# Kernel optimization log

Hardware: AMD Instinct MI355X
Metric: run time of the kernel (lower is better)

## Reference

```python
import jax, jax.numpy as jnp
import numpy as np

N = 50000      # nodes
E = 800000     # edges
F_IN = 128     # input_dim
H = 4          # GAT heads
C = 32         # hidden_dim (per head)
HC = H * C     # 128, concat GAT output
NG = 64        # graphs in batch
OUT = 10       # classes


def _gat_conv(x, src, dst, W, att_src, att_dst, bias):
    # PyG GATConv (concat=True, add_self_loops=True, negative_slope=0.2)
    n = x.shape[0]
    h = (x @ W).reshape(n, H, -1)                      # [N,H,C]
    a_s = (h * att_src).sum(-1)                        # [N,H]
    a_d = (h * att_dst).sum(-1)                        # [N,H]
    loop = jnp.arange(n)
    s = jnp.concatenate([src, loop])                   # self-loops appended
    d = jnp.concatenate([dst, loop])
    e = jax.nn.leaky_relu(a_s[s] + a_d[d], 0.2)        # [E+N,H]
    m = jax.ops.segment_max(e, d, num_segments=n)
    e = jnp.exp(e - m[d])
    z = jax.ops.segment_sum(e, d, num_segments=n)
    alpha = e / (z[d] + 1e-16)                         # edge softmax per dst,head
    out = jax.ops.segment_sum(h[s] * alpha[..., None], d, num_segments=n)
    return out.reshape(n, -1) + bias                   # [N,H*C]


def setup_inputs() -> dict:
    key = jax.random.key(0)
    ks = jax.random.split(key, 20)
    g = lambda k, shp, fan: jax.random.normal(k, shp, jnp.float32) / np.sqrt(fan)
    inp = {
        'x': jax.random.normal(ks[0], (N, F_IN), jnp.float32),
        'edge_index': jax.random.randint(ks[1], (2, E), 0, N),
        'batch': jnp.sort(jax.random.randint(ks[2], (N,), 0, NG)),
        # GATConv 1: F_IN -> H*C
        'W1': g(ks[3], (F_IN, HC), F_IN),
        'as1': g(ks[4], (H, C), C), 'ad1': g(ks[5], (H, C), C),
        'b1': jnp.zeros((HC,), jnp.float32),
        # GATConv 2: H*C -> H*C
        'W2': g(ks[6], (HC, HC), HC),
        'as2': g(ks[7], (H, C), C), 'ad2': g(ks[8], (H, C), C),
        'b2': jnp.zeros((HC,), jnp.float32),
        # GraphConv: H*C -> C  (lin_rel has bias, lin_root does not)
        'W3r': g(ks[9], (HC, C), HC), 'W3l': g(ks[10], (HC, C), HC),
        'b3': jnp.zeros((C,), jnp.float32),
        # SAGEConv: C -> C (mean aggr; lin_l has bias, lin_r does not)
        'W4l': g(ks[11], (C, C), C), 'b4l': jnp.zeros((C,), jnp.float32),
        'W4r': g(ks[12], (C, C), C),
        # MLP head
        'Wf1': g(ks[13], (C, C), C), 'bf1': jnp.zeros((C,), jnp.float32),
        'Wf2': g(ks[14], (C, OUT), C), 'bf2': jnp.zeros((OUT,), jnp.float32),
    }
    return inp


def reference(x, edge_index, batch, W1, as1, ad1, b1, W2, as2, ad2, b2,
              W3r, W3l, b3, W4l, b4l, W4r, Wf1, bf1, Wf2, bf2):
    src, dst = edge_index[0], edge_index[1]
    relu = jax.nn.relu
    n = x.shape[0]
    # GAT layers (dropout is identity in eval)
    x = relu(_gat_conv(x, src, dst, W1, as1, ad1, b1))
    x = relu(_gat_conv(x, src, dst, W2, as2, ad2, b2))
    # GraphConv: lin_rel(sum_neighbors) + lin_root(x)
    agg = jax.ops.segment_sum(x[src], dst, num_segments=n)
    x = relu(agg @ W3r + b3 + x @ W3l)
    # SAGEConv: lin_l(mean_neighbors) + lin_r(x)
    deg = jax.ops.segment_sum(jnp.ones((src.shape[0],), x.dtype), dst, num_segments=n)
    mean = jax.ops.segment_sum(x[src], dst, num_segments=n) / jnp.maximum(deg, 1.0)[:, None]
    x = relu(mean @ W4l + b4l + x @ W4r)
    # global mean pool over graphs
    cnt = jax.ops.segment_sum(jnp.ones((n,), x.dtype), batch, num_segments=NG)
    gpool = jax.ops.segment_sum(x, batch, num_segments=NG) / jnp.maximum(cnt, 1.0)[:, None]
    gpool = relu(gpool @ Wf1 + bf1)
    return gpool @ Wf2 + bf2
```

## Files before the change

### kernel.cpp

```cpp
#include <hip/hip_runtime.h>
#include <hip/hip_bf16.h>
#include <type_traits>


typedef __bf16 v8bf __attribute__((ext_vector_type(8)));
typedef float  v4f  __attribute__((ext_vector_type(4)));

__device__ __forceinline__ float lrelu(float x) { return x > 0.f ? x : 0.2f * x; }

__device__ __forceinline__ unsigned short f2bf(float f) {
    unsigned u = __float_as_uint(f);
    unsigned r = (u + 0x7FFF + ((u >> 16) & 1)) >> 16;
    return (unsigned short)r;
}
__device__ __forceinline__ float bfbits2f(unsigned short u) {
    return __uint_as_float((unsigned)u << 16);
}
__device__ __forceinline__ float bflo(int v) { return __uint_as_float((unsigned)v << 16); }
__device__ __forceinline__ float bfhi(int v) { return __uint_as_float((unsigned)v & 0xffff0000u); }
__device__ __forceinline__ int packbf2(float a, float b) {
    return (int)f2bf(a) | ((int)f2bf(b) << 16);
}

__device__ __forceinline__ void fma8(float* acc, int4 u, float w) {
    acc[0] += w * bflo(u.x); acc[1] += w * bfhi(u.x);
    acc[2] += w * bflo(u.y); acc[3] += w * bfhi(u.y);
    acc[4] += w * bflo(u.z); acc[5] += w * bfhi(u.z);
    acc[6] += w * bflo(u.w); acc[7] += w * bfhi(u.w);
}


__global__ __launch_bounds__(256) void bucket_hist(const int* __restrict__ dst,
                                                   int* __restrict__ bcount,
                                                   int E, int nbuck) {
    __shared__ int hist[256];
    int t = threadIdx.x;
    for (int i = t; i < nbuck; i += 256) hist[i] = 0;
    __syncthreads();
    int base = blockIdx.x * 4096;
    #pragma unroll
    for (int k = 0; k < 16; ++k) {
        int e = base + k * 256 + t;
        if (e < E) atomicAdd(&hist[dst[e] >> 8], 1);
    }
    __syncthreads();
    for (int i = t; i < nbuck; i += 256) {
        int c = hist[i];
        if (c) atomicAdd(&bcount[i], c);
    }
}

__global__ __launch_bounds__(256) void scan_convert(
    const int* __restrict__ bcount, int* __restrict__ bbase, int* __restrict__ gcursor,
    int nbuck, int E, int* __restrict__ rowptr, int n,
    const float* __restrict__ W1, const float* __restrict__ W2,
    const float* __restrict__ W3r, const float* __restrict__ W3l,
    const float* __restrict__ as1, const float* __restrict__ ad1,
    const float* __restrict__ as2, const float* __restrict__ ad2,
    __hip_bfloat16* __restrict__ W1t, __hip_bfloat16* __restrict__ W2t,
    __hip_bfloat16* __restrict__ W3rt, __hip_bfloat16* __restrict__ W3lt)
{
    int t = threadIdx.x;
    if (blockIdx.x == 0) {
        __shared__ int red[256];
        int v = (t < nbuck) ? bcount[t] : 0;
        red[t] = v;
        __syncthreads();
        for (int off = 1; off < 256; off <<= 1) {
            int u = (t >= off) ? red[t - off] : 0;
            __syncthreads();
            red[t] += u;
            __syncthreads();
        }
        int ex = red[t] - v;
        if (t < nbuck) { bbase[t] = ex; gcursor[t] = ex; }
        if (t == 0) { bbase[nbuck] = E; rowptr[n] = E; }
        return;
    }
    int b = blockIdx.x - 1;
    int i = b * 256 + t;
    {
        int k = i >> 7, c = i & 127;
        *(unsigned short*)&W1t[c * 128 + k] = f2bf(W1[i]);
        *(unsigned short*)&W2t[c * 128 + k] = f2bf(W2[i]);
    }
    if (i < 4096) {
        int k = i >> 5, c = i & 31;
        *(unsigned short*)&W3rt[c * 128 + k] = f2bf(W3r[i]);
        *(unsigned short*)&W3lt[c * 128 + k] = f2bf(W3l[i]);
    }
    if (b == 0) {
        for (int u = t; u < 512; u += 256) {
            int k = u & 127, hd = u >> 7;
            float vs1 = 0.f, vd1 = 0.f, vs2 = 0.f, vd2 = 0.f;
            #pragma unroll
            for (int j = 0; j < 32; ++j) {
                int c = hd * 32 + j;
                float w1 = W1[k * 128 + c], w2 = W2[k * 128 + c];
                vs1 += w1 * as1[c]; vd1 += w1 * ad1[c];
                vs2 += w2 * as2[c]; vd2 += w2 * ad2[c];
            }
            unsigned short h1s = f2bf(vs1), h1d = f2bf(vd1);
            unsigned short h2s = f2bf(vs2), h2d = f2bf(vd2);
            *(unsigned short*)&W1t[(128 + hd) * 128 + k] = h1s;
            *(unsigned short*)&W1t[(132 + hd) * 128 + k] = f2bf(vs1 - bfbits2f(h1s));
            *(unsigned short*)&W1t[(136 + hd) * 128 + k] = h1d;
            *(unsigned short*)&W1t[(140 + hd) * 128 + k] = f2bf(vd1 - bfbits2f(h1d));
            *(unsigned short*)&W2t[(128 + hd) * 128 + k] = h2s;
            *(unsigned short*)&W2t[(132 + hd) * 128 + k] = f2bf(vs2 - bfbits2f(h2s));
            *(unsigned short*)&W2t[(136 + hd) * 128 + k] = h2d;
            *(unsigned short*)&W2t[(140 + hd) * 128 + k] = f2bf(vd2 - bfbits2f(h2d));
        }
    }
}

__global__ __launch_bounds__(256) void bucket_scatter(const int* __restrict__ dst,
                                                      const int* __restrict__ src,
                                                      int* __restrict__ gcursor,
                                                      int* __restrict__ pairs,
                                                      int E, int nbuck) {
    __shared__ int hist[256], lcur[256];
    int t = threadIdx.x;
    for (int i = t; i < nbuck; i += 256) hist[i] = 0;
    __syncthreads();
    int base = blockIdx.x * 2048;
    int dreg[8];
    #pragma unroll
    for (int k = 0; k < 8; ++k) {
        int e = base + k * 256 + t;
        int d = (e < E) ? dst[e] : -1;
        dreg[k] = d;
        if (d >= 0) atomicAdd(&hist[d >> 8], 1);
    }
    __syncthreads();
    for (int i = t; i < nbuck; i += 256) {
        int c = hist[i];
        lcur[i] = c ? atomicAdd(&gcursor[i], c) : 0;
    }
    __syncthreads();
    #pragma unroll
    for (int k = 0; k < 8; ++k) {
        int e = base + k * 256 + t;
        if (e < E) {
            int d = dreg[k];
            int p = atomicAdd(&lcur[d >> 8], 1);
            pairs[p] = ((d & 255) << 17) | src[e];
        }
    }
}

__global__ __launch_bounds__(256) void bucket_fill(const int* __restrict__ pairs,
                                                   const int* __restrict__ bbase,
                                                   int* __restrict__ rowptr,
                                                   int* __restrict__ colsrc, int n) {
    __shared__ int deg[256], excl[256], cur[256];
    int b = blockIdx.x, t = threadIdx.x;
    int e0 = bbase[b], e1 = bbase[b + 1];
    int d0 = b << 8;
    deg[t] = 0;
    __syncthreads();
    for (int j = e0 + t; j < e1; j += 256)
        atomicAdd(&deg[pairs[j] >> 17], 1);
    __syncthreads();
    int v = deg[t];
    excl[t] = v;
    __syncthreads();
    for (int off = 1; off < 256; off <<= 1) {
        int u = (t >= off) ? excl[t - off] : 0;
        __syncthreads();
        excl[t] += u;
        __syncthreads();
    }
    int base = e0 + excl[t] - v;
    if (d0 + t < n) rowptr[d0 + t] = base;
    cur[t] = base;
    __syncthreads();
    for (int j = e0 + t; j < e1; j += 256) {
        int w = pairs[j];
        int p = atomicAdd(&cur[w >> 17], 1);
        colsrc[p] = w & 0x1FFFF;
    }
}

template <typename T>
__global__ __launch_bounds__(256) void gemm_att_mfma(
    const T* __restrict__ X, const __hip_bfloat16* __restrict__ Wt,
    __hip_bfloat16* __restrict__ h, float* __restrict__ a_s, float* __restrict__ a_d, int n)
{
    __shared__ __align__(16) __hip_bfloat16 sWt[144 * 136];
    int t = threadIdx.x;
    for (int i = t; i < 144 * 16; i += 256) {
        int row = i >> 4, chh = i & 15;
        *(int4*)&sWt[row * 136 + chh * 8] = *(const int4*)&Wt[row * 128 + chh * 8];
    }
    __syncthreads();
    int wave = t >> 6, lane = t & 63, quad = lane >> 4, l16 = lane & 15;

    v8bf z;
    #pragma unroll
    for (int i = 0; i < 8; ++i) z[i] = (__bf16)0.f;

    int nrb = (n + 15) >> 4;
    for (int rb = blockIdx.x * 4 + wave; rb < nrb; rb += gridDim.x * 4) {
        int rowbase = rb * 16;
        int arow = rowbase + l16;
        bool ok = arow < n;
        v8bf af[4];
        if constexpr (std::is_same<T, float>::value) {
            const float* xf = X + (size_t)(ok ? arow : 0) * 128;
            #pragma unroll
            for (int ks = 0; ks < 4; ++ks) {
                if (ok) {
                    float4 u = *(const float4*)&xf[ks * 32 + quad * 8];
                    float4 v = *(const float4*)&xf[ks * 32 + quad * 8 + 4];
                    v8bf a;
                    unsigned short r;
                    r = f2bf(u.x); a[0] = *(__bf16*)&r;
                    r = f2bf(u.y); a[1] = *(__bf16*)&r;
                    r = f2bf(u.z); a[2] = *(__bf16*)&r;
                    r = f2bf(u.w); a[3] = *(__bf16*)&r;
                    r = f2bf(v.x); a[4] = *(__bf16*)&r;
                    r = f2bf(v.y); a[5] = *(__bf16*)&r;
                    r = f2bf(v.z); a[6] = *(__bf16*)&r;
                    r = f2bf(v.w); a[7] = *(__bf16*)&r;
                    af[ks] = a;
                } else af[ks] = z;
            }
        } else {
            const v8bf* px = (const v8bf*)(X + (size_t)(ok ? arow : 0) * 128);
            #pragma unroll
            for (int ks = 0; ks < 4; ++ks) af[ks] = ok ? px[ks * 4 + quad] : z;
        }

        v4f acc[9];
        #pragma unroll
        for (int ct = 0; ct < 9; ++ct) acc[ct] = (v4f){0.f, 0.f, 0.f, 0.f};
        #pragma unroll
        for (int ct = 0; ct < 9; ++ct) {
            #pragma unroll
            for (int ks = 0; ks < 4; ++ks) {
                v8bf b = *(const v8bf*)&sWt[(ct * 16 + l16) * 136 + ks * 32 + quad * 8];
                acc[ct] = __builtin_amdgcn_mfma_f32_16x16x32_bf16(af[ks], b, acc[ct], 0, 0, 0);
            }
        }

        #pragma unroll
        for (int reg = 0; reg < 4; ++reg) {
            int r = rowbase + quad * 4 + reg;
            if (r < n) {
                #pragma unroll
                for (int ct = 0; ct < 8; ++ct)
                    *(unsigned short*)&h[(size_t)r * 128 + ct * 16 + l16] = f2bf(acc[ct][reg]);
            }
        }
        #pragma unroll
        for (int reg = 0; reg < 4; ++reg) {
            float v = acc[8][reg] + __shfl_xor(acc[8][reg], 4);
            int r = rowbase + quad * 4 + reg;
            if (r < n) {
                if (l16 < 4)                    a_s[r * 4 + l16] = v;
                else if (l16 >= 8 && l16 < 12)  a_d[r * 4 + (l16 - 8)] = v;
            }
        }
    }
}

__global__ __launch_bounds__(256) void gat_aggr(
    const __hip_bfloat16* __restrict__ h, const float* __restrict__ a_s,
    const float* __restrict__ a_d,
    const int* __restrict__ rowptr, const int* __restrict__ colsrc,
    const float* __restrict__ bias, __hip_bfloat16* __restrict__ out, int n)
{
    __shared__ float s_w[4][4 * 16 * 4];
    int t = threadIdx.x;
    int wave = t >> 6, lane = t & 63;
    int q = lane >> 4, l16 = lane & 15;
    int d = blockIdx.x * 16 + wave * 4 + q;
    if (d >= n) d = n - 1;
    int beg = rowptr[d];
    int cnt = rowptr[d + 1] - beg;
    int cm = max(cnt, __shfl_xor(cnt, 16));
    cm = max(cm, __shfl_xor(cm, 32));
    float4 ad4 = *(const float4*)&a_d[d * 4];
    float4 asd = *(const float4*)&a_s[d * 4];

    int ch = l16 * 8;
    int head = l16 >> 2;
    const char* hb = (const char*)h;
    unsigned chb = (unsigned)(ch << 1);
    int sbase = q * 64;
    int lbase = q * 16;

    float acc[8];
    #pragma unroll
    for (int i = 0; i < 8; ++i) acc[i] = 0.f;
    float zp = 0.f;

    for (int j0 = 0; j0 < cm; j0 += 16) {
        int ne = cnt - j0;
        float w0 = 0.f, w1 = 0.f, w2 = 0.f, w3 = 0.f;
        int s = 0;
        if (l16 < ne) {
            s = colsrc[beg + j0 + l16];
            float4 sv = *(const float4*)&a_s[s * 4];
            w0 = __expf(lrelu(sv.x + ad4.x));
            w1 = __expf(lrelu(sv.y + ad4.y));
            w2 = __expf(lrelu(sv.z + ad4.z));
            w3 = __expf(lrelu(sv.w + ad4.w));
        }
        float4 wv = {w0, w1, w2, w3};
        *(float4*)&s_w[wave][sbase + l16 * 4] = wv;
        __asm volatile("s_waitcnt lgkmcnt(0)" ::: "memory");
        int nemax = cm - j0; if (nemax > 16) nemax = 16;
        int k = 0;
        for (; k + 8 <= nemax; k += 8) {
            int   ss[8];
            float wj[8];
            int4  u[8];
            #pragma unroll
            for (int p2 = 0; p2 < 8; ++p2) {
                ss[p2] = __shfl(s, lbase + k + p2);
                wj[p2] = s_w[wave][sbase + (k + p2) * 4 + head];
            }
            #pragma unroll
            for (int p2 = 0; p2 < 8; ++p2)
                u[p2] = *(const int4*)(hb + (((unsigned)ss[p2] << 8) + chb));
            #pragma unroll
            for (int p2 = 0; p2 < 8; ++p2) { zp += wj[p2]; fma8(acc, u[p2], wj[p2]); }
        }
        for (; k + 4 <= nemax; k += 4) {
            int ss0 = __shfl(s, lbase + k);
            int ss1 = __shfl(s, lbase + k + 1);
            int ss2 = __shfl(s, lbase + k + 2);
            int ss3 = __shfl(s, lbase + k + 3);
            float wj0 = s_w[wave][sbase + k * 4 + head];
            float wj1 = s_w[wave][sbase + (k + 1) * 4 + head];
            float wj2 = s_w[wave][sbase + (k + 2) * 4 + head];
            float wj3 = s_w[wave][sbase + (k + 3) * 4 + head];
            int4 u0 = *(const int4*)(hb + (((unsigned)ss0 << 8) + chb));
            int4 u1 = *(const int4*)(hb + (((unsigned)ss1 << 8) + chb));
            int4 u2 = *(const int4*)(hb + (((unsigned)ss2 << 8) + chb));
            int4 u3 = *(const int4*)(hb + (((unsigned)ss3 << 8) + chb));
            zp += (wj0 + wj1) + (wj2 + wj3);
            fma8(acc, u0, wj0);
            fma8(acc, u1, wj1);
            fma8(acc, u2, wj2);
            fma8(acc, u3, wj3);
        }
        for (; k < nemax; ++k) {
            int ss0 = __shfl(s, lbase + k);
            float wj0 = s_w[wave][sbase + k * 4 + head];
            int4 u0 = *(const int4*)(hb + (((unsigned)ss0 << 8) + chb));
            zp += wj0;
            fma8(acc, u0, wj0);
        }
    }

    int4 hu = *(const int4*)(hb + (((unsigned)d << 8) + chb));
    float4 b0 = *(const float4*)&bias[ch];
    float4 b1 = *(const float4*)&bias[ch + 4];
    float eh0 = lrelu(asd.x + ad4.x), eh1 = lrelu(asd.y + ad4.y);
    float eh2 = lrelu(asd.z + ad4.z), eh3 = lrelu(asd.w + ad4.w);
    float eh = (head < 2) ? (head == 0 ? eh0 : eh1) : (head == 2 ? eh2 : eh3);
    float ws = __expf(eh);
    float inv = 1.f / (zp + ws + 1e-16f);
    float hs[8] = {bflo(hu.x), bfhi(hu.x), bflo(hu.y), bfhi(hu.y),
                   bflo(hu.z), bfhi(hu.z), bflo(hu.w), bfhi(hu.w)};
    float o[8];
    o[0] = fmaxf((acc[0] + ws * hs[0]) * inv + b0.x, 0.f);
    o[1] = fmaxf((acc[1] + ws * hs[1]) * inv + b0.y, 0.f);
    o[2] = fmaxf((acc[2] + ws * hs[2]) * inv + b0.z, 0.f);
    o[3] = fmaxf((acc[3] + ws * hs[3]) * inv + b0.w, 0.f);
    o[4] = fmaxf((acc[4] + ws * hs[4]) * inv + b1.x, 0.f);
    o[5] = fmaxf((acc[5] + ws * hs[5]) * inv + b1.y, 0.f);
    o[6] = fmaxf((acc[6] + ws * hs[6]) * inv + b1.z, 0.f);
    o[7] = fmaxf((acc[7] + ws * hs[7]) * inv + b1.w, 0.f);
    int4 ou;
    ou.x = packbf2(o[0], o[1]); ou.y = packbf2(o[2], o[3]);
    ou.z = packbf2(o[4], o[5]); ou.w = packbf2(o[6], o[7]);
    *(int4*)&out[(size_t)d * 128 + ch] = ou;
}

__global__ __launch_bounds__(256) void graphconv_lin(
    const __hip_bfloat16* __restrict__ Xb,
    const __hip_bfloat16* __restrict__ Wrt, const __hip_bfloat16* __restrict__ Wlt,
    const float* __restrict__ bias, __hip_bfloat16* __restrict__ y,
    float* __restrict__ root, int n)
{
    __shared__ __align__(16) __hip_bfloat16 sWr[32 * 136], sWl[32 * 136];
    int t = threadIdx.x;
    for (int i = t; i < 32 * 16; i += 256) {
        int row = i >> 4, chh = i & 15;
        *(int4*)&sWr[row * 136 + chh * 8] = *(const int4*)&Wrt[row * 128 + chh * 8];
        *(int4*)&sWl[row * 136 + chh * 8] = *(const int4*)&Wlt[row * 128 + chh * 8];
    }
    __syncthreads();
    int wave = t >> 6, lane = t & 63, quad = lane >> 4, l16 = lane & 15;

    v8bf z;
    #pragma unroll
    for (int i = 0; i < 8; ++i) z[i] = (__bf16)0.f;

    int nrb = (n + 15) >> 4;
    for (int rb = blockIdx.x * 4 + wave; rb < nrb; rb += gridDim.x * 4) {
        int rowbase = rb * 16;
        int arow = rowbase + l16;
        bool ok = arow < n;
        const v8bf* px = (const v8bf*)(Xb + (size_t)(ok ? arow : 0) * 128);
        v8bf fx[4];
        #pragma unroll
        for (int ks = 0; ks < 4; ++ks) fx[ks] = ok ? px[ks * 4 + quad] : z;

        v4f accR[2], accL[2];
        #pragma unroll
        for (int ct = 0; ct < 2; ++ct) {
            accR[ct] = (v4f){0.f, 0.f, 0.f, 0.f};
            accL[ct] = (v4f){0.f, 0.f, 0.f, 0.f};
            #pragma unroll
            for (int ks = 0; ks < 4; ++ks) {
                v8bf br = *(const v8bf*)&sWr[(ct * 16 + l16) * 136 + ks * 32 + quad * 8];
                accR[ct] = __builtin_amdgcn_mfma_f32_16x16x32_bf16(fx[ks], br, accR[ct], 0, 0, 0);
                v8bf bl = *(const v8bf*)&sWl[(ct * 16 + l16) * 136 + ks * 32 + quad * 8];
                accL[ct] = __builtin_amdgcn_mfma_f32_16x16x32_bf16(fx[ks], bl, accL[ct], 0, 0, 0);
            }
        }
        #pragma unroll
        for (int ct = 0; ct < 2; ++ct) {
            float bcol = bias[ct * 16 + l16];
            #pragma unroll
            for (int reg = 0; reg < 4; ++reg) {
                int r = rowbase + quad * 4 + reg;
                if (r < n) {
                    *(unsigned short*)&y[(size_t)r * 32 + ct * 16 + l16] = f2bf(accR[ct][reg]);
                    root[(size_t)r * 32 + ct * 16 + l16] = accL[ct][reg] + bcol;
                }
            }
        }
    }
}

__global__ __launch_bounds__(256) void graphconv_aggr(
    const __hip_bfloat16* __restrict__ y, const float* __restrict__ root,
    const int* __restrict__ rowptr, const int* __restrict__ colsrc,
    __hip_bfloat16* __restrict__ x3, int n)
{
    int t = threadIdx.x;
    int wave = t >> 6, lane = t & 63;
    int oct = lane >> 3, ol = lane & 7;
    int d = blockIdx.x * 32 + wave * 8 + oct;
    if (d >= n) d = n - 1;
    int beg = rowptr[d];
    int cnt = rowptr[d + 1] - beg;
    int cm = max(cnt, __shfl_xor(cnt, 8));
    cm = max(cm, __shfl_xor(cm, 16));
    cm = max(cm, __shfl_xor(cm, 32));
    int l4 = ol & 3, egrp = ol >> 2;
    int ch = l4 * 8;
    int lbase = oct * 8;
    float acc[8];
    #pragma unroll
    for (int i = 0; i < 8; ++i) acc[i] = 0.f;
    for (int j0 = 0; j0 < cm; j0 += 8) {
        int ne = cnt - j0;
        int s = (ol < ne) ? colsrc[beg + j0 + ol] : 0;
        int nemax = cm - j0; if (nemax > 8) nemax = 8;
        int kmax = (nemax + 1) >> 1;
        int k = 0;
        for (; k + 2 <= kmax; k += 2) {
            int ja = egrp + 2 * k, jb = ja + 2;
            int sa = __shfl(s, lbase + ja);
            int sb = __shfl(s, lbase + jb);
            float ma = (ja < ne) ? 1.f : 0.f;
            float mb = (jb < ne) ? 1.f : 0.f;
            int4 ua = *(const int4*)&y[(size_t)sa * 32 + ch];
            int4 ub = *(const int4*)&y[(size_t)sb * 32 + ch];
            fma8(acc, ua, ma);
            fma8(acc, ub, mb);
        }
        if (k < kmax) {
            int ja = egrp + 2 * k;
            int sa = __shfl(s, lbase + ja);
            float ma = (ja < ne) ? 1.f : 0.f;
            int4 ua = *(const int4*)&y[(size_t)sa * 32 + ch];
            fma8(acc, ua, ma);
        }
    }
    float4 r0 = {0.f, 0.f, 0.f, 0.f}, r1 = {0.f, 0.f, 0.f, 0.f};
    if (egrp == 0) {
        r0 = *(const float4*)&root[(size_t)d * 32 + ch];
        r1 = *(const float4*)&root[(size_t)d * 32 + ch + 4];
    }
    #pragma unroll
    for (int i = 0; i < 8; ++i) acc[i] += __shfl_xor(acc[i], 4);
    if (egrp == 0) {
        float o[8];
        o[0] = fmaxf(acc[0] + r0.x, 0.f); o[1] = fmaxf(acc[1] + r0.y, 0.f);
        o[2] = fmaxf(acc[2] + r0.z, 0.f); o[3] = fmaxf(acc[3] + r0.w, 0.f);
        o[4] = fmaxf(acc[4] + r1.x, 0.f); o[5] = fmaxf(acc[5] + r1.y, 0.f);
        o[6] = fmaxf(acc[6] + r1.z, 0.f); o[7] = fmaxf(acc[7] + r1.w, 0.f);
        int4 ou;
        ou.x = packbf2(o[0], o[1]); ou.y = packbf2(o[2], o[3]);
        ou.z = packbf2(o[4], o[5]); ou.w = packbf2(o[6], o[7]);
        *(int4*)&x3[(size_t)d * 32 + ch] = ou;
    }
}

__global__ __launch_bounds__(256) void sage_fused(
    const __hip_bfloat16* __restrict__ x3, const int* __restrict__ rowptr,
    const int* __restrict__ colsrc,
    const float* __restrict__ Wl, const float* __restrict__ bl,
    const float* __restrict__ Wr,
    const int* __restrict__ batch, float* __restrict__ gpool, int n)
{
    __shared__ __align__(16) float sWl[32 * 32], sWr[32 * 32];
    __shared__ __align__(16) float smean[32 * 32], sx[32 * 32];
    __shared__ float sacc[64 * 32];
    __shared__ int sbat[32];
    int t = threadIdx.x;
    int row0 = blockIdx.x * 32;
    for (int i = t; i < 1024; i += 256) {
        sWl[i] = Wl[i]; sWr[i] = Wr[i];
    }
    for (int i = t; i < 2048; i += 256) sacc[i] = 0.f;
    if (t < 32) sbat[t] = batch[min(row0 + t, n - 1)];

    int wave = t >> 6, lane = t & 63;
    int oct = lane >> 3, ol = lane & 7;
    int slot = wave * 8 + oct;
    int d = row0 + slot;
    if (d >= n) d = n - 1;
    int beg = rowptr[d];
    int cnt = rowptr[d + 1] - beg;
    int cm = max(cnt, __shfl_xor(cnt, 8));
    cm = max(cm, __shfl_xor(cm, 16));
    cm = max(cm, __shfl_xor(cm, 32));
    int l4 = ol & 3, egrp = ol >> 2;
    int ch = l4 * 8;
    int lbase = oct * 8;
    float acc[8];
    #pragma unroll
    for (int i = 0; i < 8; ++i) acc[i] = 0.f;
    for (int j0 = 0; j0 < cm; j0 += 8) {
        int ne = cnt - j0;
        int s = (ol < ne) ? colsrc[beg + j0 + ol] : 0;
        int nemax = cm - j0; if (nemax > 8) nemax = 8;
        int kmax = (nemax + 1) >> 1;
        int k = 0;
        for (; k + 2 <= kmax; k += 2) {
            int ja = egrp + 2 * k, jb = ja + 2;
            int sa = __shfl(s, lbase + ja);
            int sb = __shfl(s, lbase + jb);
            float ma = (ja < ne) ? 1.f : 0.f;
            float mb = (jb < ne) ? 1.f : 0.f;
            int4 ua = *(const int4*)&x3[(size_t)sa * 32 + ch];
            int4 ub = *(const int4*)&x3[(size_t)sb * 32 + ch];
            fma8(acc, ua, ma);
            fma8(acc, ub, mb);
        }
        if (k < kmax) {
            int ja = egrp + 2 * k;
            int sa = __shfl(s, lbase + ja);
            float ma = (ja < ne) ? 1.f : 0.f;
            int4 ua = *(const int4*)&x3[(size_t)sa * 32 + ch];
            fma8(acc, ua, ma);
        }
    }
    #pragma unroll
    for (int i = 0; i < 8; ++i) acc[i] += __shfl_xor(acc[i], 4);
    if (egrp == 0) {
        float invd = 1.f / fmaxf((float)cnt, 1.f);
        float4 lo = {acc[0] * invd, acc[1] * invd, acc[2] * invd, acc[3] * invd};
        float4 hi = {acc[4] * invd, acc[5] * invd, acc[6] * invd, acc[7] * invd};
        *(float4*)&smean[slot * 32 + ch]     = lo;
        *(float4*)&smean[slot * 32 + ch + 4] = hi;
        int4 xu = *(const int4*)&x3[(size_t)d * 32 + ch];
        float4 x0 = {bflo(xu.x), bfhi(xu.x), bflo(xu.y), bfhi(xu.y)};
        float4 x1 = {bflo(xu.z), bfhi(xu.z), bflo(xu.w), bfhi(xu.w)};
        *(float4*)&sx[slot * 32 + ch]     = x0;
        *(float4*)&sx[slot * 32 + ch + 4] = x1;
    }
    __syncthreads();

    int c = t & 31, rr = t >> 5;
    float bc = bl[c];
    int gbase = sbat[0];
    #pragma unroll
    for (int kr = 0; kr < 4; ++kr) {
        int r = rr + 8 * kr;
        float a = bc;
        const float4* pm = (const float4*)&smean[r * 32];
        const float4* px = (const float4*)&sx[r * 32];
        #pragma unroll
        for (int k4 = 0; k4 < 8; ++k4) {
            float4 vm = pm[k4], vx = px[k4];
            const float* wl = &sWl[(k4 * 4) * 32 + c];
            const float* wr = &sWr[(k4 * 4) * 32 + c];
            a += vm.x * wl[0] + vm.y * wl[32] + vm.z * wl[64] + vm.w * wl[96];
            a += vx.x * wr[0] + vx.y * wr[32] + vx.z * wr[64] + vx.w * wr[96];
        }
        float v = fmaxf(a, 0.f);
        int row = row0 + r;
        if (row < n) atomicAdd(&sacc[(sbat[r] - gbase) * 32 + c], v);
    }
    __syncthreads();
    int ngr = sbat[31] - gbase + 1;
    for (int i = t; i < ngr * 32; i += 256) {
        float v = sacc[i];
        if (v != 0.f) atomicAdd(&gpool[(size_t)gbase * 32 + i], v);
    }
}

__device__ __forceinline__ int lower_bound_i(const int* a, int n, int key) {
    int lo = 0, hi = n;
    while (lo < hi) { int mid = (lo + hi) >> 1; if (a[mid] < key) lo = mid + 1; else hi = mid; }
    return lo;
}

__global__ __launch_bounds__(256) void head_kernel(
    const float* __restrict__ gpool, const int* __restrict__ batch, int n,
    const float* __restrict__ Wf1, const float* __restrict__ bf1,
    const float* __restrict__ Wf2, const float* __restrict__ bf2, float* __restrict__ out)
{
    __shared__ float sg[64 * 32], st[64 * 32];
    __shared__ float sW1[32 * 32], sW2[32 * 10];
    __shared__ float sinv[64];
    int t = threadIdx.x;
    if (t < 64) {
        int lo = lower_bound_i(batch, n, t);
        int hi = lower_bound_i(batch, n, t + 1);
        sinv[t] = 1.f / fmaxf((float)(hi - lo), 1.f);
    }
    for (int i = t; i < 1024; i += 256) sW1[i] = Wf1[i];
    for (int i = t; i < 320; i += 256) sW2[i] = Wf2[i];
    __syncthreads();
    for (int i = t; i < 2048; i += 256) sg[i] = gpool[i] * sinv[i >> 5];
    __syncthreads();
    for (int i = t; i < 2048; i += 256) {
        int g = i >> 5, c = i & 31;
        float acc = bf1[c];
        #pragma unroll
        for (int k = 0; k < 32; ++k) acc += sg[g * 32 + k] * sW1[k * 32 + c];
        st[i] = fmaxf(acc, 0.f);
    }
    __syncthreads();
    for (int i = t; i < 640; i += 256) {
        int g = i / 10, o = i - g * 10;
        float acc = bf2[o];
        #pragma unroll
        for (int k = 0; k < 32; ++k) acc += st[g * 32 + k] * sW2[k * 10 + o];
        out[i] = acc;
    }
}

extern "C" void kernel_launch(void* const* d_in, const int* in_sizes, int n_in,
                              void* d_out, int out_size, void* d_ws, size_t ws_size,
                              hipStream_t stream) {
    const float* x    = (const float*)d_in[0];
    const int*   ei   = (const int*)d_in[1];
    const int*   batch= (const int*)d_in[2];
    const float* W1   = (const float*)d_in[3];
    const float* as1  = (const float*)d_in[4];
    const float* ad1  = (const float*)d_in[5];
    const float* b1   = (const float*)d_in[6];
    const float* W2   = (const float*)d_in[7];
    const float* as2  = (const float*)d_in[8];
    const float* ad2  = (const float*)d_in[9];
    const float* b2   = (const float*)d_in[10];
    const float* W3r  = (const float*)d_in[11];
    const float* W3l  = (const float*)d_in[12];
    const float* b3   = (const float*)d_in[13];
    const float* W4l  = (const float*)d_in[14];
    const float* b4l  = (const float*)d_in[15];
    const float* W4r  = (const float*)d_in[16];
    const float* Wf1  = (const float*)d_in[17];
    const float* bf1  = (const float*)d_in[18];
    const float* Wf2  = (const float*)d_in[19];
    const float* bf2  = (const float*)d_in[20];

    const int N = in_sizes[0] / 128;
    const int E = in_sizes[1] / 2;
    const int* src = ei;
    const int* dst = ei + E;

    char* p = (char*)d_ws;
    auto alloc = [&](size_t bytes) -> void* {
        void* r = (void*)p;
        p += (bytes + 255) & ~(size_t)255;
        return r;
    };
    __hip_bfloat16* buf1 = (__hip_bfloat16*)alloc((size_t)N * 128 * 2);
    __hip_bfloat16* buf2 = (__hip_bfloat16*)alloc((size_t)N * 128 * 2);
    __hip_bfloat16* buf3 = (__hip_bfloat16*)alloc((size_t)N * 128 * 2);
    float* aS     = (float*)alloc((size_t)N * 4 * 4);
    float* aD     = (float*)alloc((size_t)N * 4 * 4);
    int*   rowptr = (int*)alloc((size_t)(N + 1) * 4);
    int*   colsrc = (int*)alloc((size_t)E * 4);
    int*   bcount = (int*)alloc(256 * 4);
    int*   bbase  = (int*)alloc(257 * 4);
    int*   gcursor= (int*)alloc(256 * 4);
    __hip_bfloat16* W1t  = (__hip_bfloat16*)alloc(144 * 128 * 2);
    __hip_bfloat16* W2t  = (__hip_bfloat16*)alloc(144 * 128 * 2);
    __hip_bfloat16* W3rt = (__hip_bfloat16*)alloc(32 * 128 * 2);
    __hip_bfloat16* W3lt = (__hip_bfloat16*)alloc(32 * 128 * 2);
    float* gpool  = (float*)alloc(64 * 32 * 4);

    __hip_bfloat16* X3b  = buf2;
    __hip_bfloat16* Y32  = buf3;
    float*          ROOT = (float*)((char*)buf3 + (((size_t)N * 32 * 2 + 255) & ~(size_t)255));
    int*            pairs = (int*)buf3;

    const int nbuck = (N + 255) >> 8;

    hipMemsetAsync(bcount, 0, 256 * 4, stream);
    hipMemsetAsync(gpool, 0, 64 * 32 * 4, stream);
    bucket_hist<<<(E + 4095) / 4096, 256, 0, stream>>>(dst, bcount, E, nbuck);
    scan_convert<<<65, 256, 0, stream>>>(bcount, bbase, gcursor, nbuck, E, rowptr, N,
                                         W1, W2, W3r, W3l, as1, ad1, as2, ad2,
                                         W1t, W2t, W3rt, W3lt);
    bucket_scatter<<<(E + 2047) / 2048, 256, 0, stream>>>(dst, src, gcursor, pairs, E, nbuck);
    bucket_fill<<<nbuck, 256, 0, stream>>>(pairs, bbase, rowptr, colsrc, N);

    int gmm = (N + 63) / 64;
    if (gmm > 320) gmm = 320;
    const int gag4  = (N + 15) / 16;
    const int gag8  = (N + 31) / 32;
    gemm_att_mfma<float><<<gmm, 256, 0, stream>>>(x, W1t, buf3, aS, aD, N);
    gat_aggr<<<gag4, 256, 0, stream>>>(buf3, aS, aD, rowptr, colsrc, b1, buf2, N);
    gemm_att_mfma<__hip_bfloat16><<<gmm, 256, 0, stream>>>(buf2, W2t, buf3, aS, aD, N);
    gat_aggr<<<gag4, 256, 0, stream>>>(buf3, aS, aD, rowptr, colsrc, b2, buf1, N);
    graphconv_lin<<<gmm, 256, 0, stream>>>(buf1, W3rt, W3lt, b3, Y32, ROOT, N);
    graphconv_aggr<<<gag8, 256, 0, stream>>>(Y32, ROOT, rowptr, colsrc, X3b, N);
    sage_fused<<<gag8, 256, 0, stream>>>(X3b, rowptr, colsrc, W4l, b4l, W4r,
                                         batch, gpool, N);
    head_kernel<<<1, 256, 0, stream>>>(gpool, batch, N, Wf1, bf1, Wf2, bf2, (float*)d_out);
}
```

Baseline: 311.4 us.

## Cut launches: fold memsets and weight conversion into histogram, fuse head into SAGE

Drops both memset launches by having block 0 of the histogram kernel zero gpool and a completion counter. Weight conversion moves into that histogram kernel, and per-block histograms go to global memory to be summed by a single-block scan instead of global atomics. The head MLP now runs in the last-finishing block of sage_fused, detected with a threadfence plus atomic counter, which removes one more launch. The cost is a serial reduction over about 196 per-block histograms in the scan kernel and a tail of serial work in one block.

```diff
diff --git a/kernel.cpp b/kernel.cpp
--- a/kernel.cpp
+++ b/kernel.cpp
@@ -30,29 +30,9 @@
 }
 
 
-__global__ __launch_bounds__(256) void bucket_hist(const int* __restrict__ dst,
-                                                   int* __restrict__ bcount,
-                                                   int E, int nbuck) {
-    __shared__ int hist[256];
-    int t = threadIdx.x;
-    for (int i = t; i < nbuck; i += 256) hist[i] = 0;
-    __syncthreads();
-    int base = blockIdx.x * 4096;
-    #pragma unroll
-    for (int k = 0; k < 16; ++k) {
-        int e = base + k * 256 + t;
-        if (e < E) atomicAdd(&hist[dst[e] >> 8], 1);
-    }
-    __syncthreads();
-    for (int i = t; i < nbuck; i += 256) {
-        int c = hist[i];
-        if (c) atomicAdd(&bcount[i], c);
-    }
-}
-
-__global__ __launch_bounds__(256) void scan_convert(
-    const int* __restrict__ bcount, int* __restrict__ bbase, int* __restrict__ gcursor,
-    int nbuck, int E, int* __restrict__ rowptr, int n,
+__global__ __launch_bounds__(256) void bucket_hist(
+    const int* __restrict__ dst, int* __restrict__ histg, int E, int nbuck,
+    float* __restrict__ gpool, int* __restrict__ dcounter,
     const float* __restrict__ W1, const float* __restrict__ W2,
     const float* __restrict__ W3r, const float* __restrict__ W3l,
     const float* __restrict__ as1, const float* __restrict__ ad1,
@@ -60,58 +40,83 @@
     __hip_bfloat16* __restrict__ W1t, __hip_bfloat16* __restrict__ W2t,
     __hip_bfloat16* __restrict__ W3rt, __hip_bfloat16* __restrict__ W3lt)
 {
+    __shared__ int hist[256];
     int t = threadIdx.x;
+    hist[t] = 0;
+    __syncthreads();
+    int base = blockIdx.x * 4096;
+    #pragma unroll
+    for (int k = 0; k < 16; ++k) {
+        int e = base + k * 256 + t;
+        if (e < E) atomicAdd(&hist[dst[e] >> 8], 1);
+    }
+    __syncthreads();
+    histg[blockIdx.x * 256 + t] = hist[t];
+
     if (blockIdx.x == 0) {
-        __shared__ int red[256];
-        int v = (t < nbuck) ? bcount[t] : 0;
-        red[t] = v;
+        for (int i = t; i < 64 * 32; i += 256) gpool[i] = 0.f;
+        if (t == 0) *dcounter = 0;
+    }
+    if (blockIdx.x >= 1 && blockIdx.x <= 64) {
+        int b = blockIdx.x - 1;
+        int i = b * 256 + t;
+        {
+            int k = i >> 7, c = i & 127;
+            *(unsigned short*)&W1t[c * 128 + k] = f2bf(W1[i]);
+            *(unsigned short*)&W2t[c * 128 + k] = f2bf(W2[i]);
+        }
+        if (i < 4096) {
+            int k = i >> 5, c = i & 31;
+            *(unsigned short*)&W3rt[c * 128 + k] = f2bf(W3r[i]);
+            *(unsigned short*)&W3lt[c * 128 + k] = f2bf(W3l[i]);
+        }
+        if (b == 0) {
+            for (int u = t; u < 512; u += 256) {
+                int k = u & 127, hd = u >> 7;
+                float vs1 = 0.f, vd1 = 0.f, vs2 = 0.f, vd2 = 0.f;
+                #pragma unroll
+                for (int j = 0; j < 32; ++j) {
+                    int c = hd * 32 + j;
+                    float w1 = W1[k * 128 + c], w2 = W2[k * 128 + c];
+                    vs1 += w1 * as1[c]; vd1 += w1 * ad1[c];
+                    vs2 += w2 * as2[c]; vd2 += w2 * ad2[c];
+                }
+                unsigned short h1s = f2bf(vs1), h1d = f2bf(vd1);
+                unsigned short h2s = f2bf(vs2), h2d = f2bf(vd2);
+                *(unsigned short*)&W1t[(128 + hd) * 128 + k] = h1s;
+                *(unsigned short*)&W1t[(132 + hd) * 128 + k] = f2bf(vs1 - bfbits2f(h1s));
+                *(unsigned short*)&W1t[(136 + hd) * 128 + k] = h1d;
+                *(unsigned short*)&W1t[(140 + hd) * 128 + k] = f2bf(vd1 - bfbits2f(h1d));
+                *(unsigned short*)&W2t[(128 + hd) * 128 + k] = h2s;
+                *(unsigned short*)&W2t[(132 + hd) * 128 + k] = f2bf(vs2 - bfbits2f(h2s));
+                *(unsigned short*)&W2t[(136 + hd) * 128 + k] = h2d;
+                *(unsigned short*)&W2t[(140 + hd) * 128 + k] = f2bf(vd2 - bfbits2f(h2d));
+            }
+        }
+    }
+}
+
+__global__ __launch_bounds__(256) void scan_kernel(
+    const int* __restrict__ histg, int nblkh,
+    int* __restrict__ bbase, int* __restrict__ gcursor,
+    int nbuck, int E, int* __restrict__ rowptr, int n)
+{
+    __shared__ int red[256];
+    int t = threadIdx.x;
+    int v = 0;
+    for (int b = 0; b < nblkh; ++b) v += histg[b * 256 + t];
+    if (t >= nbuck) v = 0;
+    red[t] = v;
+    __syncthreads();
+    for (int off = 1; off < 256; off <<= 1) {
+        int u = (t >= off) ? red[t - off] : 0;
         __syncthreads();
-        for (int off = 1; off < 256; off <<= 1) {
-            int u = (t >= off) ? red[t - off] : 0;
-            __syncthreads();
-            red[t] += u;
-            __syncthreads();
-        }
-        int ex = red[t] - v;
-        if (t < nbuck) { bbase[t] = ex; gcursor[t] = ex; }
-        if (t == 0) { bbase[nbuck] = E; rowptr[n] = E; }
-        return;
-    }
-    int b = blockIdx.x - 1;
-    int i = b * 256 + t;
-    {
-        int k = i >> 7, c = i & 127;
-        *(unsigned short*)&W1t[c * 128 + k] = f2bf(W1[i]);
-        *(unsigned short*)&W2t[c * 128 + k] = f2bf(W2[i]);
-    }
-    if (i < 4096) {
-        int k = i >> 5, c = i & 31;
-        *(unsigned short*)&W3rt[c * 128 + k] = f2bf(W3r[i]);
-        *(unsigned short*)&W3lt[c * 128 + k] = f2bf(W3l[i]);
-    }
-    if (b == 0) {
-        for (int u = t; u < 512; u += 256) {
-            int k = u & 127, hd = u >> 7;
-            float vs1 = 0.f, vd1 = 0.f, vs2 = 0.f, vd2 = 0.f;
-            #pragma unroll
-            for (int j = 0; j < 32; ++j) {
-                int c = hd * 32 + j;
-                float w1 = W1[k * 128 + c], w2 = W2[k * 128 + c];
-                vs1 += w1 * as1[c]; vd1 += w1 * ad1[c];
-                vs2 += w2 * as2[c]; vd2 += w2 * ad2[c];
-            }
-            unsigned short h1s = f2bf(vs1), h1d = f2bf(vd1);
-            unsigned short h2s = f2bf(vs2), h2d = f2bf(vd2);
-            *(unsigned short*)&W1t[(128 + hd) * 128 + k] = h1s;
-            *(unsigned short*)&W1t[(132 + hd) * 128 + k] = f2bf(vs1 - bfbits2f(h1s));
-            *(unsigned short*)&W1t[(136 + hd) * 128 + k] = h1d;
-            *(unsigned short*)&W1t[(140 + hd) * 128 + k] = f2bf(vd1 - bfbits2f(h1d));
-            *(unsigned short*)&W2t[(128 + hd) * 128 + k] = h2s;
-            *(unsigned short*)&W2t[(132 + hd) * 128 + k] = f2bf(vs2 - bfbits2f(h2s));
-            *(unsigned short*)&W2t[(136 + hd) * 128 + k] = h2d;
-            *(unsigned short*)&W2t[(140 + hd) * 128 + k] = f2bf(vd2 - bfbits2f(h2d));
-        }
-    }
+        red[t] += u;
+        __syncthreads();
+    }
+    int ex = red[t] - v;
+    if (t < nbuck) { bbase[t] = ex; gcursor[t] = ex; }
+    if (t == 0) { bbase[nbuck] = E; rowptr[n] = E; }
 }
 
 __global__ __launch_bounds__(256) void bucket_scatter(const int* __restrict__ dst,
@@ -505,17 +510,30 @@
     }
 }
 
+__device__ __forceinline__ int lower_bound_i(const int* a, int n, int key) {
+    int lo = 0, hi = n;
+    while (lo < hi) { int mid = (lo + hi) >> 1; if (a[mid] < key) lo = mid + 1; else hi = mid; }
+    return lo;
+}
+
 __global__ __launch_bounds__(256) void sage_fused(
     const __hip_bfloat16* __restrict__ x3, const int* __restrict__ rowptr,
     const int* __restrict__ colsrc,
     const float* __restrict__ Wl, const float* __restrict__ bl,
     const float* __restrict__ Wr,
-    const int* __restrict__ batch, float* __restrict__ gpool, int n)
+    const int* __restrict__ batch, float* __restrict__ gpool, int n,
+    const float* __restrict__ Wf1, const float* __restrict__ bf1,
+    const float* __restrict__ Wf2, const float* __restrict__ bf2,
+    float* __restrict__ out, int* __restrict__ dcounter)
 {
-    __shared__ __align__(16) float sWl[32 * 32], sWr[32 * 32];
-    __shared__ __align__(16) float smean[32 * 32], sx[32 * 32];
-    __shared__ float sacc[64 * 32];
+    __shared__ __align__(16) float lds[6144];
     __shared__ int sbat[32];
+    __shared__ int slast;
+    float* sWl   = lds;
+    float* sWr   = lds + 1024;
+    float* smean = lds + 2048;
+    float* sx    = lds + 3072;
+    float* sacc  = lds + 4096;
     int t = threadIdx.x;
     int row0 = blockIdx.x * 32;
     for (int i = t; i < 1024; i += 256) {
@@ -608,23 +626,17 @@
         float v = sacc[i];
         if (v != 0.f) atomicAdd(&gpool[(size_t)gbase * 32 + i], v);
     }
-}
-
-__device__ __forceinline__ int lower_bound_i(const int* a, int n, int key) {
-    int lo = 0, hi = n;
-    while (lo < hi) { int mid = (lo + hi) >> 1; if (a[mid] < key) lo = mid + 1; else hi = mid; }
-    return lo;
-}
-
-__global__ __launch_bounds__(256) void head_kernel(
-    const float* __restrict__ gpool, const int* __restrict__ batch, int n,
-    const float* __restrict__ Wf1, const float* __restrict__ bf1,
-    const float* __restrict__ Wf2, const float* __restrict__ bf2, float* __restrict__ out)
-{
-    __shared__ float sg[64 * 32], st[64 * 32];
-    __shared__ float sW1[32 * 32], sW2[32 * 10];
-    __shared__ float sinv[64];
-    int t = threadIdx.x;
+
+    __threadfence();
+    if (t == 0) slast = (atomicAdd(dcounter, 1) == (int)gridDim.x - 1) ? 1 : 0;
+    __syncthreads();
+    if (!slast) return;
+    __threadfence();
+    float* sg   = lds;
+    float* st   = lds + 2048;
+    float* sW1  = lds + 4096;
+    float* sW2  = lds + 5120;
+    float* sinv = lds + 5440;
     if (t < 64) {
         int lo = lower_bound_i(batch, n, t);
         int hi = lower_bound_i(batch, n, t + 1);
@@ -633,22 +645,22 @@
     for (int i = t; i < 1024; i += 256) sW1[i] = Wf1[i];
     for (int i = t; i < 320; i += 256) sW2[i] = Wf2[i];
     __syncthreads();
-    for (int i = t; i < 2048; i += 256) sg[i] = gpool[i] * sinv[i >> 5];
+    for (int i = t; i < 2048; i += 256) sg[i] = atomicAdd(&gpool[i], 0.f) * sinv[i >> 5];
     __syncthreads();
     for (int i = t; i < 2048; i += 256) {
-        int g = i >> 5, c = i & 31;
-        float acc = bf1[c];
-        #pragma unroll
-        for (int k = 0; k < 32; ++k) acc += sg[g * 32 + k] * sW1[k * 32 + c];
-        st[i] = fmaxf(acc, 0.f);
+        int g = i >> 5, cc = i & 31;
+        float a = bf1[cc];
+        #pragma unroll
+        for (int k = 0; k < 32; ++k) a += sg[g * 32 + k] * sW1[k * 32 + cc];
+        st[i] = fmaxf(a, 0.f);
     }
     __syncthreads();
     for (int i = t; i < 640; i += 256) {
         int g = i / 10, o = i - g * 10;
-        float acc = bf2[o];
-        #pragma unroll
-        for (int k = 0; k < 32; ++k) acc += st[g * 32 + k] * sW2[k * 10 + o];
-        out[i] = acc;
+        float a = bf2[o];
+        #pragma unroll
+        for (int k = 0; k < 32; ++k) a += st[g * 32 + k] * sW2[k * 10 + o];
+        out[i] = a;
     }
 }
 
@@ -695,15 +707,19 @@
     float* aD     = (float*)alloc((size_t)N * 4 * 4);
     int*   rowptr = (int*)alloc((size_t)(N + 1) * 4);
     int*   colsrc = (int*)alloc((size_t)E * 4);
-    int*   bcount = (int*)alloc(256 * 4);
     int*   bbase  = (int*)alloc(257 * 4);
     int*   gcursor= (int*)alloc(256 * 4);
+    int*   dcounter=(int*)alloc(4);
     __hip_bfloat16* W1t  = (__hip_bfloat16*)alloc(144 * 128 * 2);
     __hip_bfloat16* W2t  = (__hip_bfloat16*)alloc(144 * 128 * 2);
     __hip_bfloat16* W3rt = (__hip_bfloat16*)alloc(32 * 128 * 2);
     __hip_bfloat16* W3lt = (__hip_bfloat16*)alloc(32 * 128 * 2);
     float* gpool  = (float*)alloc(64 * 32 * 4);
 
+    int nblkh = (E + 4095) / 4096;
+    if (nblkh < 65) nblkh = 65;
+    int* histg = (int*)alloc((size_t)nblkh * 256 * 4);
+
     __hip_bfloat16* X3b  = buf2;
     __hip_bfloat16* Y32  = buf3;
     float*          ROOT = (float*)((char*)buf3 + (((size_t)N * 32 * 2 + 255) & ~(size_t)255));
@@ -711,12 +727,10 @@
 
     const int nbuck = (N + 255) >> 8;
 
-    hipMemsetAsync(bcount, 0, 256 * 4, stream);
-    hipMemsetAsync(gpool, 0, 64 * 32 * 4, stream);
-    bucket_hist<<<(E + 4095) / 4096, 256, 0, stream>>>(dst, bcount, E, nbuck);
-    scan_convert<<<65, 256, 0, stream>>>(bcount, bbase, gcursor, nbuck, E, rowptr, N,
-                                         W1, W2, W3r, W3l, as1, ad1, as2, ad2,
-                                         W1t, W2t, W3rt, W3lt);
+    bucket_hist<<<nblkh, 256, 0, stream>>>(dst, histg, E, nbuck, gpool, dcounter,
+                                           W1, W2, W3r, W3l, as1, ad1, as2, ad2,
+                                           W1t, W2t, W3rt, W3lt);
+    scan_kernel<<<1, 256, 0, stream>>>(histg, nblkh, bbase, gcursor, nbuck, E, rowptr, N);
     bucket_scatter<<<(E + 2047) / 2048, 256, 0, stream>>>(dst, src, gcursor, pairs, E, nbuck);
     bucket_fill<<<nbuck, 256, 0, stream>>>(pairs, bbase, rowptr, colsrc, N);
 
@@ -731,6 +745,6 @@
     graphconv_lin<<<gmm, 256, 0, stream>>>(buf1, W3rt, W3lt, b3, Y32, ROOT, N);
     graphconv_aggr<<<gag8, 256, 0, stream>>>(Y32, ROOT, rowptr, colsrc, X3b, N);
     sage_fused<<<gag8, 256, 0, stream>>>(X3b, rowptr, colsrc, W4l, b4l, W4r,
-                                         batch, gpool, N);
-    head_kernel<<<1, 256, 0, stream>>>(gpool, batch, N, Wf1, bf1, Wf2, bf2, (float*)d_out);
-}
+                                         batch, gpool, N,
+                                         Wf1, bf1, Wf2, bf2, (float*)d_out, dcounter);
+}
```

Measured after the change: 413.0 us. 32.6% more time.
